# Kernel tuning notes

Measured on AMD Instinct MI355X. Metric: run time of the kernel, lower is better.

Reference implementation:

```python
import jax, jax.numpy as jnp
import numpy as np

NUM_BINS = 16


def _luma(x):
    # x: [B, 3, H, W] -> [B, H, W]
    return 0.299 * x[:, 0] + 0.587 * x[:, 1] + 0.114 * x[:, 2]


def setup_inputs() -> dict:
    key = jax.random.key(0)
    k1, k2, k3 = jax.random.split(key, 3)
    shape = (16, 3, 512, 512)
    pred = jax.random.uniform(k1, shape, dtype=jnp.float32)
    target = jax.random.uniform(k2, shape, dtype=jnp.float32)
    input_img = jax.random.uniform(k3, shape, dtype=jnp.float32)
    return {"pred": pred, "target": target, "input_img": input_img}


def reference(pred, target, input_img):
    nb = NUM_BINS
    pl = _luma(pred).ravel()
    tl = _luma(target).ravel()
    il = _luma(input_img).ravel()
    # bin i covers [i/nb, (i+1)/nb); values >= 1.0 fall in NO bin in the
    # original loop, so route them to an extra segment that is discarded.
    bins = jnp.clip(jnp.floor(il * nb).astype(jnp.int32), 0, nb - 1)
    bins = jnp.where(il >= 1.0, nb, bins)
    ones = jnp.ones_like(il)
    counts = jax.ops.segment_sum(ones, bins, num_segments=nb + 1)[:nb]
    psum = jax.ops.segment_sum(pl, bins, num_segments=nb + 1)[:nb]
    tsum = jax.ops.segment_sum(tl, bins, num_segments=nb + 1)[:nb]
    safe = jnp.maximum(counts, 1.0)
    per_bin = jnp.where(counts > 0, jnp.abs(psum / safe - tsum / safe), 0.0)
    return jnp.sum(per_bin) / nb
```

## Files before the change

kernel.cpp:

```cpp
#include <hip/hip_runtime.h>
#include <hip/hip_bf16.h>


#define CH4 65536
#define NBINS 16
#define NCOL 32

typedef float f4 __attribute__((ext_vector_type(4)));

__device__ __forceinline__ float luma_exact(float r, float g, float b) {
    return __fadd_rn(__fadd_rn(__fmul_rn(0.299f, r), __fmul_rn(0.587f, g)),
                     __fmul_rn(0.114f, b));
}

__global__ __launch_bounds__(256) void tm_stage1(
    const f4* __restrict__ pred, const f4* __restrict__ target,
    const f4* __restrict__ input,
    float* __restrict__ partials,
    int G, int rows)
{
    __shared__ float dsh[NBINS * 256];
    __shared__ unsigned long long cl[256], ch[256];
    const int t = threadIdx.x;

    #pragma unroll
    for (int k = 0; k < NBINS; ++k) dsh[k * 256 + t] = 0.0f;
    __syncthreads();

    unsigned long long cLo = 0ULL, cHi = 0ULL;

    const int T = gridDim.x * 256;
    for (int g0 = blockIdx.x * 256 + t; g0 < G; g0 += 2 * T) {
        const int g1 = g0 + T;
        const bool ok1 = (g1 < G);
        const int a0 = (g0 >> 16) * (3 * CH4) + (g0 & (CH4 - 1));
        const int a1 = ok1 ? (g1 >> 16) * (3 * CH4) + (g1 & (CH4 - 1)) : a0;

        const f4 iA0 = input[a0];
        const f4 iA1 = input[a0 + CH4];
        const f4 iA2 = input[a0 + 2 * CH4];
        const f4 iB0 = input[a1];
        const f4 iB1 = input[a1 + CH4];
        const f4 iB2 = input[a1 + 2 * CH4];

        unsigned bpack = 0u, excl = ok1 ? 0u : 0xF0u;
        #pragma unroll
        for (int j = 0; j < 4; ++j) {
            const float ilA = luma_exact(iA0[j], iA1[j], iA2[j]);
            int bA = (int)floorf(__fmul_rn(ilA, 16.0f));
            bA = min(max(bA, 0), NBINS - 1);
            bpack |= (unsigned)bA << (4 * j);
            excl |= (ilA >= 1.0f ? 1u : 0u) << j;

            const float ilB = luma_exact(iB0[j], iB1[j], iB2[j]);
            int bB = (int)floorf(__fmul_rn(ilB, 16.0f));
            bB = min(max(bB, 0), NBINS - 1);
            bpack |= (unsigned)bB << (4 * (j + 4));
            excl |= (ilB >= 1.0f ? 1u : 0u) << (j + 4);
        }

        const f4 pA0 = pred[a0];
        const f4 pA1 = pred[a0 + CH4];
        const f4 pA2 = pred[a0 + 2 * CH4];
        const f4 pB0 = pred[a1];
        const f4 pB1 = pred[a1 + CH4];
        const f4 pB2 = pred[a1 + 2 * CH4];
        float pl[8];
        #pragma unroll
        for (int j = 0; j < 4; ++j) {
            pl[j]     = luma_exact(pA0[j], pA1[j], pA2[j]);
            pl[j + 4] = luma_exact(pB0[j], pB1[j], pB2[j]);
        }

        const f4 tA0 = target[a0];
        const f4 tA1 = target[a0 + CH4];
        const f4 tA2 = target[a0 + 2 * CH4];
        const f4 tB0 = target[a1];
        const f4 tB1 = target[a1 + CH4];
        const f4 tB2 = target[a1 + 2 * CH4];

        #pragma unroll
        for (int j = 0; j < 4; ++j) {
            {
                const float tlA = luma_exact(tA0[j], tA1[j], tA2[j]);
                if (!((excl >> j) & 1u)) {
                    const int b = (int)((bpack >> (4 * j)) & 0xFu);
                    dsh[b * 256 + t] += pl[j] - tlA;
                    const unsigned long long inc = 1ULL << ((b & 7) * 8);
                    if (b < 8) cLo += inc; else cHi += inc;
                }
            }
            {
                const float tlB = luma_exact(tB0[j], tB1[j], tB2[j]);
                if (!((excl >> (j + 4)) & 1u)) {
                    const int b = (int)((bpack >> (4 * (j + 4))) & 0xFu);
                    dsh[b * 256 + t] += pl[j + 4] - tlB;
                    const unsigned long long inc = 1ULL << ((b & 7) * 8);
                    if (b < 8) cLo += inc; else cHi += inc;
                }
            }
        }
    }

    cl[t] = cLo; ch[t] = cHi;
    __syncthreads();

    const int b = t >> 4, l = t & 15;
    float s = 0.0f; int c = 0;
    #pragma unroll
    for (int k = 0; k < 16; ++k) {
        s += dsh[b * 256 + k * 16 + l];
        const unsigned long long packed = (b < 8) ? cl[k * 16 + l] : ch[k * 16 + l];
        c += (int)((packed >> ((b & 7) * 8)) & 0xFFULL);
    }
    #pragma unroll
    for (int k = 8; k; k >>= 1) {
        s += __shfl_down(s, k, 16);
        c += __shfl_down(c, k, 16);
    }
    if (l == 0) {
        partials[b * rows + blockIdx.x] = (float)c;
        partials[(NBINS + b) * rows + blockIdx.x] = s;
    }
}

__global__ __launch_bounds__(512) void tm_stage2(
    const float4* __restrict__ partials4,
    float* __restrict__ out, int rows4)
{
    __shared__ double col[NCOL];
    const int t = threadIdx.x;
    const int c = t >> 4;
    const int l = t & 15;

    double s = 0.0;
    for (int k = l; k < rows4; k += 16) {
        const float4 v = partials4[c * rows4 + k];
        s += (double)v.x + (double)v.y + (double)v.z + (double)v.w;
    }
    #pragma unroll
    for (int k = 8; k; k >>= 1) s += __shfl_down(s, k, 16);
    if (l == 0) col[c] = s;
    __syncthreads();

    if (t == 0) {
        double acc = 0.0;
        #pragma unroll
        for (int i = 0; i < NBINS; ++i) {
            const double cnt = col[i];
            if (cnt > 0.0) acc += fabs(col[NBINS + i]) / cnt;
        }
        out[0] = (float)(acc / (double)NBINS);
    }
}

extern "C" void kernel_launch(void* const* d_in, const int* in_sizes, int n_in,
                              void* d_out, int out_size, void* d_ws, size_t ws_size,
                              hipStream_t stream) {
    const float* pred   = (const float*)d_in[0];
    const float* target = (const float*)d_in[1];
    const float* input  = (const float*)d_in[2];

    const int G = in_sizes[0] / 12;

    int blocks = 2048;
    const size_t maxRows = ws_size / (NCOL * sizeof(float));
    if ((size_t)blocks > maxRows) blocks = (int)maxRows;
    if (blocks < 1) blocks = 1;
    const int rows = (blocks + 3) & ~3;
    float* partials = (float*)d_ws;

    tm_stage1<<<blocks, 256, 0, stream>>>(
        (const f4*)pred, (const f4*)target, (const f4*)input,
        partials, G, rows);
    tm_stage2<<<1, 512, 0, stream>>>(
        (const float4*)partials, (float*)d_out, rows / 4);
}
```

Before: 42.61 us.

## Split into bin-map kernel and per-channel accumulation kernel

```diff
diff --git a/kernel.cpp b/kernel.cpp
--- a/kernel.cpp
+++ b/kernel.cpp
@@ -4,7 +4,7 @@
 
 #define CH4 65536
 #define NBINS 16
-#define NCOL 32
+#define NCOLS 64
 
 typedef float f4 __attribute__((ext_vector_type(4)));
 
@@ -13,122 +13,109 @@
                      __fmul_rn(0.114f, b));
 }
 
-__global__ __launch_bounds__(256) void tm_stage1(
-    const f4* __restrict__ pred, const f4* __restrict__ target,
-    const f4* __restrict__ input,
-    float* __restrict__ partials,
-    int G, int rows)
+__global__ __launch_bounds__(256) void k1_bins(
+    const f4* __restrict__ input, unsigned* __restrict__ binmap,
+    float* __restrict__ partials, int G, int rows)
 {
-    __shared__ float dsh[NBINS * 256];
     __shared__ unsigned long long cl[256], ch[256];
     const int t = threadIdx.x;
-
-    #pragma unroll
-    for (int k = 0; k < NBINS; ++k) dsh[k * 256 + t] = 0.0f;
-    __syncthreads();
-
     unsigned long long cLo = 0ULL, cHi = 0ULL;
 
-    const int T = gridDim.x * 256;
-    for (int g0 = blockIdx.x * 256 + t; g0 < G; g0 += 2 * T) {
-        const int g1 = g0 + T;
-        const bool ok1 = (g1 < G);
-        const int a0 = (g0 >> 16) * (3 * CH4) + (g0 & (CH4 - 1));
-        const int a1 = ok1 ? (g1 >> 16) * (3 * CH4) + (g1 & (CH4 - 1)) : a0;
-
-        const f4 iA0 = input[a0];
-        const f4 iA1 = input[a0 + CH4];
-        const f4 iA2 = input[a0 + 2 * CH4];
-        const f4 iB0 = input[a1];
-        const f4 iB1 = input[a1 + CH4];
-        const f4 iB2 = input[a1 + 2 * CH4];
-
-        unsigned bpack = 0u, excl = ok1 ? 0u : 0xF0u;
+    const int stride = gridDim.x * 512;
+    for (long long base = (long long)blockIdx.x * 512; base < G; base += stride) {
         #pragma unroll
-        for (int j = 0; j < 4; ++j) {
-            const float ilA = luma_exact(iA0[j], iA1[j], iA2[j]);
-            int bA = (int)floorf(__fmul_rn(ilA, 16.0f));
-            bA = min(max(bA, 0), NBINS - 1);
-            bpack |= (unsigned)bA << (4 * j);
-            excl |= (ilA >= 1.0f ? 1u : 0u) << j;
-
-            const float ilB = luma_exact(iB0[j], iB1[j], iB2[j]);
-            int bB = (int)floorf(__fmul_rn(ilB, 16.0f));
-            bB = min(max(bB, 0), NBINS - 1);
-            bpack |= (unsigned)bB << (4 * (j + 4));
-            excl |= (ilB >= 1.0f ? 1u : 0u) << (j + 4);
-        }
-
-        const f4 pA0 = pred[a0];
-        const f4 pA1 = pred[a0 + CH4];
-        const f4 pA2 = pred[a0 + 2 * CH4];
-        const f4 pB0 = pred[a1];
-        const f4 pB1 = pred[a1 + CH4];
-        const f4 pB2 = pred[a1 + 2 * CH4];
-        float pl[8];
-        #pragma unroll
-        for (int j = 0; j < 4; ++j) {
-            pl[j]     = luma_exact(pA0[j], pA1[j], pA2[j]);
-            pl[j + 4] = luma_exact(pB0[j], pB1[j], pB2[j]);
-        }
-
-        const f4 tA0 = target[a0];
-        const f4 tA1 = target[a0 + CH4];
-        const f4 tA2 = target[a0 + 2 * CH4];
-        const f4 tB0 = target[a1];
-        const f4 tB1 = target[a1 + CH4];
-        const f4 tB2 = target[a1 + 2 * CH4];
-
-        #pragma unroll
-        for (int j = 0; j < 4; ++j) {
-            {
-                const float tlA = luma_exact(tA0[j], tA1[j], tA2[j]);
-                if (!((excl >> j) & 1u)) {
-                    const int b = (int)((bpack >> (4 * j)) & 0xFu);
-                    dsh[b * 256 + t] += pl[j] - tlA;
-                    const unsigned long long inc = 1ULL << ((b & 7) * 8);
-                    if (b < 8) cLo += inc; else cHi += inc;
+        for (int half = 0; half < 2; ++half) {
+            const int g = (int)base + half * 256 + t;
+            if (g < G) {
+                const int a = (g >> 16) * (3 * CH4) + (g & (CH4 - 1));
+                const f4 i0 = input[a];
+                const f4 i1 = input[a + CH4];
+                const f4 i2 = input[a + 2 * CH4];
+                unsigned code = 0u;
+                #pragma unroll
+                for (int j = 0; j < 4; ++j) {
+                    const float il = luma_exact(i0[j], i1[j], i2[j]);
+                    int b = (int)floorf(__fmul_rn(il, 16.0f));
+                    b = min(max(b, 0), NBINS - 1);
+                    if (il >= 1.0f) b = 16;
+                    code |= (unsigned)b << (8 * j);
+                    if (b < 16) {
+                        const unsigned long long inc = 1ULL << ((b & 7) * 8);
+                        if (b < 8) cLo += inc; else cHi += inc;
+                    }
                 }
-            }
-            {
-                const float tlB = luma_exact(tB0[j], tB1[j], tB2[j]);
-                if (!((excl >> (j + 4)) & 1u)) {
-                    const int b = (int)((bpack >> (4 * (j + 4))) & 0xFu);
-                    dsh[b * 256 + t] += pl[j + 4] - tlB;
-                    const unsigned long long inc = 1ULL << ((b & 7) * 8);
-                    if (b < 8) cLo += inc; else cHi += inc;
-                }
+                binmap[g] = code;
             }
         }
     }
 
     cl[t] = cLo; ch[t] = cHi;
     __syncthreads();
-
     const int b = t >> 4, l = t & 15;
-    float s = 0.0f; int c = 0;
+    int c = 0;
     #pragma unroll
     for (int k = 0; k < 16; ++k) {
-        s += dsh[b * 256 + k * 16 + l];
-        const unsigned long long packed = (b < 8) ? cl[k * 16 + l] : ch[k * 16 + l];
-        c += (int)((packed >> ((b & 7) * 8)) & 0xFFULL);
+        const unsigned long long p = (b < 8) ? cl[k * 16 + l] : ch[k * 16 + l];
+        c += (int)((p >> ((b & 7) * 8)) & 0xFFULL);
     }
     #pragma unroll
-    for (int k = 8; k; k >>= 1) {
-        s += __shfl_down(s, k, 16);
-        c += __shfl_down(c, k, 16);
-    }
-    if (l == 0) {
-        partials[b * rows + blockIdx.x] = (float)c;
-        partials[(NBINS + b) * rows + blockIdx.x] = s;
-    }
+    for (int k = 8; k; k >>= 1) c += __shfl_down(c, k, 16);
+    if (l == 0) partials[b * rows + blockIdx.x] = (float)c;
 }
 
-__global__ __launch_bounds__(512) void tm_stage2(
+__global__ __launch_bounds__(256) void k2_acc(
+    const f4* __restrict__ pred, const f4* __restrict__ target,
+    const unsigned* __restrict__ binmap, float* __restrict__ partials,
+    int G, int rows, int blocksPerChan)
+{
+    __shared__ float dsh[NBINS * 256];
+    const int t = threadIdx.x;
+    const int ch_ = blockIdx.x % 3;
+    const int blk = blockIdx.x / 3;
+    const float w = (ch_ == 0) ? 0.299f : ((ch_ == 1) ? 0.587f : 0.114f);
+    const int cOff = ch_ * CH4;
+
+    #pragma unroll
+    for (int k = 0; k < NBINS; ++k) dsh[k * 256 + t] = 0.0f;
+    __syncthreads();
+
+    const int stride = blocksPerChan * 512;
+    for (long long base = (long long)blk * 512; base < G; base += stride) {
+        #pragma unroll
+        for (int half = 0; half < 2; ++half) {
+            const int g = (int)base + half * 256 + t;
+            if (g < G) {
+                const int a = (g >> 16) * (3 * CH4) + cOff + (g & (CH4 - 1));
+                const f4 p  = __builtin_nontemporal_load(&pred[a]);
+                const f4 tv = __builtin_nontemporal_load(&target[a]);
+                const unsigned bm = binmap[g];
+                #pragma unroll
+                for (int j = 0; j < 4; ++j) {
+                    const int b = (int)((bm >> (8 * j)) & 0xFFu);
+                    if (b < 16)
+                        dsh[b * 256 + t] +=
+                            __fmul_rn(w, p[j]) - __fmul_rn(w, tv[j]);
+                }
+            }
+        }
+    }
+
+    __syncthreads();
+    const int b = t >> 4, l = t & 15;
+    float s = 0.0f;
+    #pragma unroll
+    for (int k = 0; k < 16; ++k) s += dsh[b * 256 + k * 16 + l];
+    #pragma unroll
+    for (int k = 8; k; k >>= 1) s += __shfl_down(s, k, 16);
+    if (l == 0)
+        partials[(NBINS + ch_ * NBINS + b) * rows + blk] = s;
+}
+
+__global__ __launch_bounds__(1024) void tm_stage2(
     const float4* __restrict__ partials4,
     float* __restrict__ out, int rows4)
 {
-    __shared__ double col[NCOL];
+    __shared__ double col[NCOLS];
     const int t = threadIdx.x;
     const int c = t >> 4;
     const int l = t & 15;
@@ -148,7 +135,11 @@
         #pragma unroll
         for (int i = 0; i < NBINS; ++i) {
             const double cnt = col[i];
-            if (cnt > 0.0) acc += fabs(col[NBINS + i]) / cnt;
+            if (cnt > 0.0) {
+                const double ds = col[NBINS + i] + col[2 * NBINS + i]
+                                + col[3 * NBINS + i];
+                acc += fabs(ds) / cnt;
+            }
         }
         out[0] = (float)(acc / (double)NBINS);
     }
@@ -163,16 +154,16 @@
 
     const int G = in_sizes[0] / 12;
 
-    int blocks = 2048;
-    const size_t maxRows = ws_size / (NCOL * sizeof(float));
-    if ((size_t)blocks > maxRows) blocks = (int)maxRows;
-    if (blocks < 1) blocks = 1;
-    const int rows = (blocks + 3) & ~3;
+    const int blocksPerChan = 2048;
+    const int rows = blocksPerChan;
     float* partials = (float*)d_ws;
+    unsigned* binmap = (unsigned*)(partials + (size_t)NCOLS * rows);
 
-    tm_stage1<<<blocks, 256, 0, stream>>>(
-        (const f4*)pred, (const f4*)target, (const f4*)input,
-        partials, G, rows);
-    tm_stage2<<<1, 512, 0, stream>>>(
+    k1_bins<<<blocksPerChan, 256, 0, stream>>>(
+        (const f4*)input, binmap, partials, G, rows);
+    k2_acc<<<3 * blocksPerChan, 256, 0, stream>>>(
+        (const f4*)pred, (const f4*)target, binmap, partials,
+        G, rows, blocksPerChan);
+    tm_stage2<<<1, 1024, 0, stream>>>(
         (const float4*)partials, (float*)d_out, rows / 4);
 }
```

After: 47.75 us. +12.1%, slower.
